# Optimization experiments

Hardware: AMD Instinct MI355X
Metric: run time of the kernel (lower is better)

The kernel has to match this reference:

```python
import jax, jax.numpy as jnp
import numpy as np
from functools import partial

IMG = 800
ANCHOR_SIZES = (32.0, 64.0, 128.0, 256.0, 512.0)
RATIOS = (0.5, 1.0, 2.0)
PRE_NMS = 1000
POST_NMS = 1000
NMS_TH = 0.7
MIN_SIZE = 1e-3
POOL = 7
SRATIO = 2  # roi_align sampling_ratio
SCALES = (0.25, 0.125, 0.0625, 0.03125)
BBOX_CLIP = float(np.log(1000.0 / 16.0))


def _cell_anchors(size):
    r = jnp.asarray(RATIOS, jnp.float32)
    hr = jnp.sqrt(r)
    wr = 1.0 / hr
    ws = size * wr
    hs = size * hr
    return jnp.round(jnp.stack([-ws / 2, -hs / 2, ws / 2, hs / 2], axis=1))  # [A,4]


def _grid_anchors(gh, gw, sh, sw, cell):
    sx = jnp.arange(gw, dtype=jnp.float32) * sw
    sy = jnp.arange(gh, dtype=jnp.float32) * sh
    yy, xx = jnp.meshgrid(sy, sx, indexing='ij')
    shifts = jnp.stack([xx, yy, xx, yy], axis=-1).reshape(-1, 4)
    # order: H-major, W, then A anchors per cell (matches torchvision)
    return (shifts[:, None, :] + cell[None, :, :]).reshape(-1, 4)


def _flatten_level(obj, dl):
    # permute_and_flatten: [B,A,H,W] -> [B,H*W*A], [B,4A,H,W] -> [B,H*W*A,4]
    B, A, H, W = obj.shape
    o = obj.transpose(0, 2, 3, 1).reshape(B, -1)
    d = dl.reshape(B, A, 4, H, W).transpose(0, 3, 4, 1, 2).reshape(B, -1, 4)
    return o, d


def _decode(deltas, anchors):
    # BoxCoder.decode with weights (1,1,1,1)
    w = anchors[:, 2] - anchors[:, 0]
    h = anchors[:, 3] - anchors[:, 1]
    cx = anchors[:, 0] + 0.5 * w
    cy = anchors[:, 1] + 0.5 * h
    dx, dy = deltas[..., 0], deltas[..., 1]
    dw = jnp.minimum(deltas[..., 2], BBOX_CLIP)
    dh = jnp.minimum(deltas[..., 3], BBOX_CLIP)
    pcx = dx * w + cx
    pcy = dy * h + cy
    pw = jnp.exp(dw) * w
    ph = jnp.exp(dh) * h
    return jnp.stack([pcx - 0.5 * pw, pcy - 0.5 * ph, pcx + 0.5 * pw, pcy + 0.5 * ph], axis=-1)


def _iou_one(box, boxes):
    a1 = (box[2] - box[0]) * (box[3] - box[1])
    a2 = (boxes[:, 2] - boxes[:, 0]) * (boxes[:, 3] - boxes[:, 1])
    lt = jnp.maximum(box[:2], boxes[:, :2])
    rb = jnp.minimum(box[2:], boxes[:, 2:])
    wh = jnp.clip(rb - lt, 0.0)
    inter = wh[:, 0] * wh[:, 1]
    return inter / (a1 + a2 - inter)


def _nms(boxes, scores, k):
    # greedy NMS, fixed k iterations (jit-friendly)
    def step(s, _):
        i = jnp.argmax(s)
        sup = _iou_one(boxes[i], boxes) > NMS_TH
        s = jnp.where(sup, -jnp.inf, s).at[i].set(-jnp.inf)
        return s, i
    _, idx = jax.lax.scan(step, scores, None, length=k)
    return idx


def _roi_align(feat, rois, scale):
    # feat [C,H,W], rois [R,4] in image coords -> [R,C,POOL,POOL]; aligned=False semantics
    C, H, W = feat.shape
    R = rois.shape[0]
    x1, y1 = rois[:, 0] * scale, rois[:, 1] * scale
    x2, y2 = rois[:, 2] * scale, rois[:, 3] * scale
    rw = jnp.maximum(x2 - x1, 1.0)
    rh = jnp.maximum(y2 - y1, 1.0)
    S = POOL * SRATIO
    t = (jnp.arange(S, dtype=jnp.float32) + 0.5) / S
    y = jnp.broadcast_to((y1[:, None] + rh[:, None] * t)[:, :, None], (R, S, S))
    x = jnp.broadcast_to((x1[:, None] + rw[:, None] * t)[:, None, :], (R, S, S))
    mask = (y >= -1.0) & (y <= H) & (x >= -1.0) & (x <= W)
    yc = jnp.clip(y, 0.0, H - 1.0)
    xc = jnp.clip(x, 0.0, W - 1.0)
    y0 = jnp.floor(yc).astype(jnp.int32)
    x0 = jnp.floor(xc).astype(jnp.int32)
    y1i = jnp.minimum(y0 + 1, H - 1)
    x1i = jnp.minimum(x0 + 1, W - 1)
    ly = yc - y0
    lx = xc - x0
    v00 = feat[:, y0, x0]
    v01 = feat[:, y0, x1i]
    v10 = feat[:, y1i, x0]
    v11 = feat[:, y1i, x1i]  # [C,R,S,S]
    val = ((1 - ly) * (1 - lx) * v00 + (1 - ly) * lx * v01 + ly * (1 - lx) * v10 + ly * lx * v11) * mask
    pooled = val.reshape(C, R, POOL, SRATIO, POOL, SRATIO).mean(axis=(3, 5))
    return pooled.transpose(1, 0, 2, 3)


def _forward(image_tensors, feats, objs, dls):
    B = image_tensors.shape[0]
    grids = [o.shape[-2:] for o in objs]
    anchors = jnp.concatenate([
        _grid_anchors(gh, gw, float(IMG // gh), float(IMG // gw), _cell_anchors(s))
        for (gh, gw), s in zip(grids, ANCHOR_SIZES)], axis=0)
    flat = [_flatten_level(o, d) for o, d in zip(objs, dls)]
    # RPN detaches both objectness and deltas before proposal filtering
    obj = jax.lax.stop_gradient(jnp.concatenate([f[0] for f in flat], axis=1))   # [B,N]
    dl = jax.lax.stop_gradient(jnp.concatenate([f[1] for f in flat], axis=1))    # [B,N,4]
    proposals = _decode(dl, anchors)                                             # [B,N,4]
    npl = [3 * gh * gw for gh, gw in grids]
    offs = np.concatenate([[0], np.cumsum(npl)])
    idx_parts, lvl_parts = [], []
    for l, n in enumerate(npl):
        k = min(PRE_NMS, n)
        _, ix = jax.lax.top_k(obj[:, offs[l]:offs[l + 1]], k)
        idx_parts.append(ix + offs[l])
        lvl_parts.append(jnp.full((k,), l, jnp.float32))
    idx = jnp.concatenate(idx_parts, axis=1)   # [B,K]
    lvl = jnp.concatenate(lvl_parts)           # [K]
    boxes = jnp.take_along_axis(proposals, idx[..., None], axis=1)
    scores = jax.nn.sigmoid(jnp.take_along_axis(obj, idx, axis=1))
    boxes = jnp.clip(boxes, 0.0, float(IMG))   # clip_boxes_to_image (square image)
    ws = boxes[..., 2] - boxes[..., 0]
    hs = boxes[..., 3] - boxes[..., 1]
    valid = (ws >= MIN_SIZE) & (hs >= MIN_SIZE)  # remove_small_boxes via score masking
    scores = jnp.where(valid, scores, -jnp.inf)
    # batched_nms: offset boxes per level so NMS is independent across levels
    off_boxes = boxes + (lvl * (IMG + 1.0))[None, :, None]
    keep = jax.vmap(lambda b, s: _nms(b, s, POST_NMS))(off_boxes, scores)  # [B,POST]
    props = jnp.take_along_axis(boxes, keep[..., None], axis=1)            # [B,POST,4]
    # MultiScaleRoIAlign level mapping (k0=4, canonical 224)
    area = (props[..., 2] - props[..., 0]) * (props[..., 3] - props[..., 1])
    li = jnp.clip(jnp.floor(4.0 + jnp.log2(jnp.sqrt(area) / 224.0 + 1e-6)), 2.0, 5.0).astype(jnp.int32) - 2
    R = props.shape[1]
    C = feats[0].shape[1]
    box_feats = jnp.zeros((B, R, C, POOL, POOL), feats[0].dtype)
    for l, (f, sc) in enumerate(zip(feats, SCALES)):
        pooled = jax.vmap(partial(_roi_align, scale=sc))(f, props)  # [B,R,C,7,7]
        box_feats = box_feats + pooled * (li == l)[..., None, None, None]
    return props, box_feats.reshape(B * R, C, POOL, POOL)


def setup_inputs() -> dict:
    key = jax.random.key(0)
    ks = jax.random.split(key, 16)
    B, C = 2, 256
    grids = [(200, 200), (100, 100), (50, 50), (25, 25), (13, 13)]
    d = {}
    d['image_tensors'] = jax.random.normal(ks[0], (B, 3, IMG, IMG), jnp.float32)
    for i in range(4):
        gh, gw = grids[i]
        d[f'features_{i}'] = jax.random.normal(ks[1 + i], (B, C, gh, gw), jnp.float32)
    for i in range(5):
        gh, gw = grids[i]
        d[f'objectness_{i}'] = jax.random.normal(ks[5 + i], (B, 3, gh, gw), jnp.float32)
        d[f'pred_bbox_deltas_{i}'] = jax.random.normal(ks[10 + i], (B, 12, gh, gw), jnp.float32)
    return d


def reference(image_tensors, features_0, features_1, features_2, features_3,
              objectness_0, objectness_1, objectness_2, objectness_3, objectness_4,
              pred_bbox_deltas_0, pred_bbox_deltas_1, pred_bbox_deltas_2,
              pred_bbox_deltas_3, pred_bbox_deltas_4):
    feats = [features_0, features_1, features_2, features_3]
    objs = [objectness_0, objectness_1, objectness_2, objectness_3, objectness_4]
    dls = [pred_bbox_deltas_0, pred_bbox_deltas_1, pred_bbox_deltas_2,
           pred_bbox_deltas_3, pred_bbox_deltas_4]
    return _forward(image_tensors, feats, objs, dls)
```

## Files before the change

kernel.cpp:

```cpp
#include <hip/hip_runtime.h>
#include <math.h>

typedef unsigned int u32;
typedef unsigned long long u64;

#define N_ALL 159882
#define NC 4507
#define MROW 72
#define NEGINF_KEY 0x007FFFFFu
#define IMGF 800.0f
#define BBOX_CLIP_F 4.135166556742356f
#define EMIT_S 16

#define NHWC_L1 10240000u
#define NHWC_L2 12800000u
#define NHWC_L3 13440000u
#define NHWC_BS 13600000u

__constant__ int   c_offs[5]  = {0,120000,150000,157500,159375};
__constant__ int   c_gw[5]    = {200,100,50,25,13};
__constant__ float c_stride[5]= {4.f,8.f,16.f,32.f,61.f};
__constant__ float c_size[5]  = {32.f,64.f,128.f,256.f,512.f};
__constant__ int   c_koff[5]  = {0,1000,2000,3000,4000};
__constant__ int   c_k[5]     = {1000,1000,1000,1000,507};
__constant__ float c_ratio[3] = {0.5f,1.f,2.f};

struct PtrArgs { const float* obj[5]; const float* dl[5]; };

__device__ __forceinline__ u32 fkey32f(float x){
  u32 u = __float_as_uint(x);
  return (u & 0x80000000u) ? ~u : (u | 0x80000000u);
}
__device__ __forceinline__ int level_of(int g){
  return (g >= 159375) ? 4 : (g >= 157500) ? 3 : (g >= 150000) ? 2 : (g >= 120000) ? 1 : 0;
}
__device__ __forceinline__ u64 readlane64(u64 v, int l){
  u32 lo = (u32)v, hi = (u32)(v >> 32);
  u32 a = (u32)__builtin_amdgcn_readlane((int)lo, l);
  u32 b = (u32)__builtin_amdgcn_readlane((int)hi, l);
  return ((u64)b << 32) | (u64)a;
}

__global__ void k_zero(u32* ghist, u32* wcnt, u32* tcnt, int B){
  int n = B*5*65536;
  int idx = blockIdx.x*blockDim.x + threadIdx.x;
  for (int i = idx; i < n; i += gridDim.x*blockDim.x) ghist[i] = 0;
  if (idx < B*5){ wcnt[idx] = 0; tcnt[idx] = 0; }
}

__global__ void k_decode(PtrArgs pa, int B, float* boxes_all, u32* key_all, u32* fkey_all,
                         u32* ghist){
#pragma clang fp contract(off)
  int idx = blockIdx.x*blockDim.x + threadIdx.x;
  int total = B*N_ALL;
  if (idx >= total) return;
  int b = idx / N_ALL;
  int g = idx - b*N_ALL;
  int l = level_of(g);
  int n = g - c_offs[l];
  int a = n % 3;
  int pos = n / 3;
  int gw = c_gw[l];
  int wx = pos % gw;
  int hy = pos / gw;
  int plane = gw*gw;
  const float* obj = pa.obj[l];
  const float* dl  = pa.dl[l];
  float logit = obj[(size_t)(b*3 + a)*plane + hy*gw + wx];
  size_t dbase = (size_t)(b*12 + a*4)*plane + (size_t)hy*gw + wx;
  float d0 = dl[dbase];
  float d1 = dl[dbase + (size_t)plane];
  float d2 = dl[dbase + (size_t)2*plane];
  float d3 = dl[dbase + (size_t)3*plane];
  float ratio = c_ratio[a];
  float hr = sqrtf(ratio);
  float wr = 1.0f/hr;
  float wsz = c_size[l]*wr;
  float hsz = c_size[l]*hr;
  float ca0 = rintf(-0.5f*wsz), ca1 = rintf(-0.5f*hsz);
  float ca2 = rintf( 0.5f*wsz), ca3 = rintf( 0.5f*hsz);
  float st = c_stride[l];
  float shx = (float)wx*st, shy = (float)hy*st;
  float ax1 = shx+ca0, ay1 = shy+ca1, ax2 = shx+ca2, ay2 = shy+ca3;
  float w = ax2-ax1, h = ay2-ay1;
  float cx = ax1 + 0.5f*w, cy = ay1 + 0.5f*h;
  float dw = fminf(d2, BBOX_CLIP_F), dh = fminf(d3, BBOX_CLIP_F);
  float pcx = d0*w + cx, pcy = d1*h + cy;
  float pw = expf(dw)*w, ph = expf(dh)*h;
  float x1 = pcx - 0.5f*pw, y1 = pcy - 0.5f*ph;
  float x2 = pcx + 0.5f*pw, y2 = pcy + 0.5f*ph;
  x1 = fminf(fmaxf(x1,0.f),IMGF); y1 = fminf(fmaxf(y1,0.f),IMGF);
  x2 = fminf(fmaxf(x2,0.f),IMGF); y2 = fminf(fmaxf(y2,0.f),IMGF);
  bool valid = ((x2-x1) >= 0.001f) && ((y2-y1) >= 0.001f);
  ((float4*)boxes_all)[idx] = make_float4(x1,y1,x2,y2);
  u32 key = fkey32f(logit);
  key_all[idx] = key;
  atomicAdd(&ghist[(size_t)(b*5 + l)*65536 + (key >> 16)], 1u);
  float sgf = 1.0f/(1.0f + expf(-logit));
  fkey_all[idx] = valid ? fkey32f(sgf) : NEGINF_KEY;
}

__global__ __launch_bounds__(1024) void k_sel(const u32* ghist, int2* meta, int B){
  int bl = blockIdx.x;
  int l = bl % 5;
  int k = c_k[l];
  const u32* h = ghist + (size_t)bl*65536;
  __shared__ u32 ssum[1024];
  __shared__ int2 s_meta;
  int tid = threadIdx.x;
  u32 cnt[64];
  u32 tot = 0;
  const uint4* h4 = (const uint4*)(h + tid*64);
  #pragma unroll
  for (int j = 0; j < 16; ++j){
    uint4 v = h4[j];
    cnt[4*j+0]=v.x; cnt[4*j+1]=v.y; cnt[4*j+2]=v.z; cnt[4*j+3]=v.w;
    tot += v.x+v.y+v.z+v.w;
  }
  ssum[tid] = tot;
  __syncthreads();
  for (int s = 1; s < 1024; s <<= 1){
    u32 v = ssum[tid] + ((tid+s < 1024) ? ssum[tid+s] : 0);
    __syncthreads(); ssum[tid] = v; __syncthreads();
  }
  u32 run = (tid+1 < 1024) ? ssum[tid+1] : 0;
  #pragma unroll
  for (int j = 63; j >= 0; --j){
    u32 cur = run + cnt[j];
    if (cur >= (u32)k && run < (u32)k){ s_meta.x = tid*64 + j; s_meta.y = (int)run; }
    run = cur;
  }
  __syncthreads();
  if (tid == 0) meta[bl] = s_meta;
}

__global__ __launch_bounds__(1024) void k_emit(const u32* key_all, const int2* meta,
                                               u32* cand_g, u32* wcnt, u32* tcnt,
                                               u64* tbuf, int B){
  int bid = blockIdx.x;
  int bl = bid / EMIT_S, c = bid - bl*EMIT_S;
  int b = bl / 5, l = bl - b*5;
  int g0 = c_offs[l];
  int N  = ((l==4)?N_ALL:c_offs[l+1]) - g0;
  int CH = (N + EMIT_S - 1)/EMIT_S;
  int st = c*CH, en = st + CH; if (en > N) en = N;
  if (st >= en) return;
  u32 bstar = (u32)meta[bl].x;
  const u32* keys = key_all + (size_t)b*N_ALL + g0;
  u32* out = cand_g + (size_t)b*NC + c_koff[l];
  u64* tb = tbuf + (size_t)bl*4096;
  int tid = threadIdx.x;
  int lane = tid & 63;
  u64 below = lane ? (~0ull >> (64 - lane)) : 0ull;
  for (int i0 = st; i0 < en; i0 += 1024){
    int i = i0 + tid;
    bool inb = (i < en);
    u32 kk = inb ? keys[i] : 0u;
    u32 bin = kk >> 16;
    bool isW = inb && (bin > bstar);
    bool isT = inb && (bin == bstar);
    u64 wb = __ballot(isW);
    if (wb){
      int wn = __popcll(wb);
      int b0 = 0;
      if (lane == 0) b0 = (int)atomicAdd(&wcnt[bl], (u32)wn);
      b0 = __shfl(b0, 0);
      if (isW) out[b0 + __popcll(wb & below)] = (u32)(g0 + i);
    }
    u64 tbm = __ballot(isT);
    if (tbm){
      int tn = __popcll(tbm);
      int b0 = 0;
      if (lane == 0) b0 = (int)atomicAdd(&tcnt[bl], (u32)tn);
      b0 = __shfl(b0, 0);
      if (isT){
        int slot = b0 + __popcll(tbm & below);
        if (slot < 4096) tb[slot] = ((u64)kk << 32) | (u32)(~(u32)(g0 + i));
      }
    }
  }
}

__global__ __launch_bounds__(1024) void k_fin(const int2* meta, const u32* tcnt,
                                              const u64* tbuf, u32* cand_g, int B){
  int bl = blockIdx.x;
  int b = bl/5, l = bl - b*5;
  int k = c_k[l];
  int chi = meta[bl].y;
  int r = k - chi;
  u32* out = cand_g + (size_t)b*NC + c_koff[l];
  __shared__ u64 buf[4096];
  int tid = threadIdx.x;
  int m = (int)tcnt[bl]; if (m > 4096) m = 4096;
  int P = 1; while (P < m) P <<= 1; if (P < 2) P = 2;
  const u64* tb = tbuf + (size_t)bl*4096;
  for (int i = tid; i < m; i += 1024) buf[i] = tb[i];
  for (int i = m + tid; i < P; i += 1024) buf[i] = 0;
  __syncthreads();
  for (u32 ksz = 2; ksz <= (u32)P; ksz <<= 1){
    for (u32 j = ksz >> 1; j > 0; j >>= 1){
      for (int i = tid; i < P; i += 1024){
        u32 ixj = (u32)i ^ j;
        if (ixj > (u32)i){
          u64 x = buf[i], y = buf[ixj];
          bool up = ((i & ksz) == 0);
          if (up ? (x < y) : (x > y)){ buf[i] = y; buf[ixj] = x; }
        }
      }
      __syncthreads();
    }
  }
  for (int t = tid; t < r && t < m; t += 1024) out[chi + t] = ~(u32)buf[t];
}

__global__ __launch_bounds__(1024) void k_rank(u32* cand_g, const u32* key_all, int B){
  int blk = blockIdx.x; int b = blk/5, l = blk - b*5;
  int k = c_k[l];
  u32* seg = cand_g + (size_t)b*NC + c_koff[l];
  __shared__ u64 sk[1024];
  int tid = threadIdx.x;
  u64 v = 0;
  if (tid < k){
    u32 g = seg[tid];
    v = ((u64)key_all[(size_t)b*N_ALL + g]<<32) | (u32)(~g);
  }
  sk[tid] = v;
  __syncthreads();
  for (u32 ksz=2;ksz<=1024;ksz<<=1){
    for (u32 j=ksz>>1;j>0;j>>=1){
      int i = tid;
      u32 ixj = (u32)i ^ j;
      if (ixj > (u32)i){
        u64 x = sk[i], y = sk[ixj];
        bool up = ((i & ksz) == 0);
        if (up ? (x < y) : (x > y)){ sk[i]=y; sk[ixj]=x; }
      }
      __syncthreads();
    }
  }
  if (tid < k) seg[tid] = ~(u32)sk[tid];
}

__device__ __forceinline__ void merge_elem(const u64* As, const u64* Bs, u64* dst,
                                           int m, int n, int k){
  int lo = k - n; if (lo < 0) lo = 0;
  int hi = (k < m) ? k : m;
  while (lo < hi){
    int mid = (lo + hi) >> 1;
    if (As[mid] > Bs[k-1-mid]) lo = mid + 1; else hi = mid;
  }
  int a = lo, bb = k - lo;
  u64 out;
  if (a < m && (bb >= n || As[a] > Bs[bb])) out = As[a]; else out = Bs[bb];
  dst[k] = out;
}

__global__ __launch_bounds__(1024) void k_sortcand(const u32* cand_g, const u32* fkey_all,
                                                   const float* boxes_all,
                                                   float* sorted_box, float* sorted_off,
                                                   u32* fcnt_ws, float* pos0box){
  __shared__ u64 sA[NC];
  __shared__ u64 sB[NC];
  __shared__ u32 wsum[16];
  __shared__ int s_f;
  int b = blockIdx.x, tid = threadIdx.x;
  int lane = tid & 63, wv = tid >> 6;
  if (tid == 0) s_f = 0;
  size_t cbase = (size_t)b*NC;
  size_t abase = (size_t)b*N_ALL;
  u64 below = lane ? (~0ull >> (64 - lane)) : 0ull;
  for (int l = 0; l < 5; ++l){
    int kl = c_k[l], ko = c_koff[l];
    bool act = tid < kl;
    u32 fk = 0; bool val = false;
    u32 i_g = (u32)(ko + tid);
    if (act){
      u32 g = cand_g[cbase + i_g];
      fk = fkey_all[abase + g];
      val = fk > NEGINF_KEY;
    }
    u64 bal = __ballot(act && val);
    int pv_w = __popcll(bal & below);
    if (lane == 0) wsum[wv] = (u32)__popcll(bal);
    __syncthreads();
    int pre = 0, Vl = 0;
    #pragma unroll
    for (int w2 = 0; w2 < 16; ++w2){
      int s = (int)wsum[w2];
      if (w2 < wv) pre += s;
      Vl += s;
    }
    if (tid == 0) s_f += Vl;
    if (act){
      int pv = pre + pv_w;
      int pos = val ? pv : (Vl + (tid - pv));
      sA[ko + pos] = ((u64)fk << 32) | (u32)(~i_g);
    }
    __syncthreads();
  }
  for (int k = tid; k < NC; k += 1024){
    if (k < 2000)       merge_elem(sA,        sA + 1000, sB,        1000, 1000, k);
    else if (k < 4000)  merge_elem(sA + 2000, sA + 3000, sB + 2000, 1000, 1000, k - 2000);
    else                sB[k] = sA[k];
  }
  __syncthreads();
  for (int k = tid; k < NC; k += 1024){
    if (k < 4000) merge_elem(sB, sB + 2000, sA, 2000, 2000, k);
    else          sA[k] = sB[k];
  }
  __syncthreads();
  for (int k = tid; k < NC; k += 1024){
    merge_elem(sA, sA + 4000, sB, 4000, 507, k);
  }
  __syncthreads();
  for (int i = tid; i < NC; i += 1024){
    u32 posc = ~(u32)sB[i];
    u32 g = cand_g[cbase + posc];
    int lvl = level_of((int)g);
    float4 bx = ((const float4*)boxes_all)[abase + g];
    ((float4*)sorted_box)[cbase + i] = bx;
    float off = 801.0f*(float)lvl;
    ((float4*)sorted_off)[cbase + i] = make_float4(bx.x+off, bx.y+off, bx.z+off, bx.w+off);
  }
  if (tid == 0){
    fcnt_ws[b] = (u32)s_f;
    u32 g0b = cand_g[cbase + 0];
    float4 bx = ((const float4*)boxes_all)[abase + g0b];
    ((float4*)pos0box)[b] = bx;
  }
}

__global__ void k_iou(const float* sorted_off, u64* M){
#pragma clang fp contract(off)
  int i = blockIdx.x, b = blockIdx.y, lane = threadIdx.x;
  const float4* boxes = ((const float4*)sorted_off) + (size_t)b*NC;
  float4 bi = boxes[i];
  float a1 = (bi.z-bi.x)*(bi.w-bi.y);
  u64* row = M + ((size_t)b*NC + i)*MROW;
  for (int w=0; w<71; w++){
    int j = w*64 + lane;
    bool sup = false;
    if (j < NC){
      float4 bj = boxes[j];
      float a2 = (bj.z-bj.x)*(bj.w-bj.y);
      float ltx = fmaxf(bi.x,bj.x), lty = fmaxf(bi.y,bj.y);
      float rbx = fminf(bi.z,bj.z), rby = fminf(bi.w,bj.w);
      float wx = fmaxf(rbx-ltx,0.f), wy = fmaxf(rby-lty,0.f);
      float inter = wx*wy;
      float iou = inter/(a1+a2-inter);
      sup = iou > 0.7f;
    }
    u64 word = __ballot(sup);
    if (lane==0) row[w] = word;
  }
}

#define GETQ2(q) { if (t2){ int jj=__builtin_ctzll(t2); t2&=t2-1; q = &buf[cb][jj*72]; } else q = zbuf; }
__global__ __launch_bounds__(256) void k_nms_tr(const float* sorted_box, const u64* M,
                      const u32* fcnt_ws, const float* pos0box, float* props, int B,
                      const float* f0, const float* f1, const float* f2, const float* f3,
                      float* nhwc, int doTr){
  __shared__ u64 buf[2][64*72];
  __shared__ u64 zbuf[72];
  __shared__ int ki[1000];
  __shared__ int s_kc, s_done;
  int bid = blockIdx.x;
  int tid = threadIdx.x;
  if (bid >= B){
    float (*t)[65] = reinterpret_cast<float(*)[65]>(&buf[0][0]);
    int id = bid - B;
    int b = id / 3328;
    int rem = id - b*3328;
    int P, W; const float* f; u32 loff;
    if (rem < 2500){ W=200; f=f0; loff=0u; }
    else if (rem < 3128){ W=100; f=f1; loff=NHWC_L1; rem -= 2500; }
    else if (rem < 3288){ W=50;  f=f2; loff=NHWC_L2; rem -= 3128; }
    else { W=25; f=f3; loff=NHWC_L3; rem -= 3288; }
    P = W*W;
    int ctile = rem & 3, ptile = rem >> 2;
    int c0 = ctile*64, p0 = ptile*64;
    const float* src = f + (size_t)b*256*P;
    float* dst = nhwc + (size_t)b*NHWC_BS + loff;
    int q   = tid & 15;
    int cl0 = tid >> 4;
    bool vec4ok = ((P & 3) == 0);
    int p = p0 + 4*q;
    float4 v[4];
    #pragma unroll
    for (int k = 0; k < 4; ++k){
      int cl = cl0 + 16*k;
      const float* s = src + (size_t)(c0+cl)*P + p;
      if (vec4ok && (p + 3 < P)){
        v[k] = *(const float4*)s;
      } else {
        v[k].x = (p   < P) ? s[0] : 0.f;
        v[k].y = (p+1 < P) ? s[1] : 0.f;
        v[k].z = (p+2 < P) ? s[2] : 0.f;
        v[k].w = (p+3 < P) ? s[3] : 0.f;
      }
    }
    #pragma unroll
    for (int k = 0; k < 4; ++k){
      int cl = cl0 + 16*k;
      t[cl][4*q+0] = v[k].x; t[cl][4*q+1] = v[k].y;
      t[cl][4*q+2] = v[k].z; t[cl][4*q+3] = v[k].w;
    }
    __syncthreads();
    #pragma unroll
    for (int k = 0; k < 4; ++k){
      int pl = cl0 + 16*k;
      int pp = p0 + pl;
      if (pp < P){
        float4 o = make_float4(t[4*q+0][pl], t[4*q+1][pl],
                               t[4*q+2][pl], t[4*q+3][pl]);
        *(float4*)(dst + (size_t)pp*256 + c0 + 4*q) = o;
      }
    }
    return;
  }
  int b = bid;
  int F = (int)fcnt_ws[b];
  const u64* Mb = M + (size_t)b*NC*MROW;
  int nch = (F + 63) >> 6;
  int lane = tid & 63, wv = tid >> 6;
  if (tid == 0){ s_kc = 0; s_done = (nch == 0) ? 1 : 0; }
  if (tid < 72) zbuf[tid] = 0ull;
  if (nch > 0){
    for (int e = tid; e < 64*72; e += 256){
      int rr = e / 72, wo = e - rr*72;
      int r2 = rr; if (r2 > NC-1) r2 = NC-1;
      buf[0][e] = Mb[(size_t)r2*MROW + wo];
    }
  }
  u64 rg[24];
  if (wv > 0 && nch > 1){
    #pragma unroll
    for (int k = 0; k < 24; ++k){
      int e = (tid - 64) + k*192;
      int rr = e/72, wo = e - rr*72;
      int r2 = 64 + rr; if (r2 > NC-1) r2 = NC-1;
      rg[k] = Mb[(size_t)r2*MROW + wo];
    }
  }
  __syncthreads();
  u64 sup0 = 0, sup1 = 0;
  int kc = 0;
  for (int c = 0; c < nch; ++c){
    int cb = c & 1;
    if (wv > 0){
      if (c + 1 < nch){
        #pragma unroll
        for (int k = 0; k < 24; ++k){
          int e = (tid - 64) + k*192;
          buf[cb^1][e] = rg[k];
        }
      }
      if (c + 2 < nch){
        int base2 = (c + 2) << 6;
        #pragma unroll
        for (int k = 0; k < 24; ++k){
          int e = (tid - 64) + k*192;
          int rr = e/72, wo = e - rr*72;
          int r2 = base2 + rr; if (r2 > NC-1) r2 = NC-1;
          rg[k] = Mb[(size_t)r2*MROW + wo];
        }
      }
    } else if (kc < 1000){
      int base = c << 6;
      int cnt = F - base; if (cnt > 64) cnt = 64;
      u64 supw = (c < 64) ? readlane64(sup0, c) : readlane64(sup1, c - 64);
      u64 alive = ~supw;
      if (cnt < 64) alive &= ((1ull << cnt) - 1ull);
      u64 wrow = buf[cb][lane*72 + c];
      u64 below = lane ? (~0ull >> (64 - lane)) : 0ull;
      u64 colb = wrow & below;
      bool myal = ((alive >> lane) & 1ull) != 0ull;
      u64 kept = __ballot(myal);
      #pragma unroll 1
      for (int it = 0; it < 64; ++it){
        bool kj = myal && ((kept & colb) == 0ull);
        u64 nk = __ballot(kj);
        if (nk == kept) break;
        kept = nk;
      }
      int cnt_k = __popcll(kept);
      int rank  = __popcll(kept & below);
      int budget = 1000 - kc;
      bool sel = ((kept >> lane) & 1ull) && (rank < budget);
      if (sel) ki[kc + rank] = base + lane;
      if (cnt_k >= budget){
        if (lane == 0){ s_done = 1; s_kc = 1000; }
      } else {
        kc += cnt_k;
        u64 t2 = kept;
        while (t2){
          const u64 *q0,*q1,*q2,*q3,*q4,*q5,*q6,*q7;
          const u64 *q8,*q9,*q10,*q11,*q12,*q13,*q14,*q15;
          GETQ2(q0) GETQ2(q1) GETQ2(q2) GETQ2(q3)
          GETQ2(q4) GETQ2(q5) GETQ2(q6) GETQ2(q7)
          GETQ2(q8) GETQ2(q9) GETQ2(q10) GETQ2(q11)
          GETQ2(q12) GETQ2(q13) GETQ2(q14) GETQ2(q15)
          u64 a0=q0[lane],a1=q1[lane],a2=q2[lane],a3=q3[lane];
          u64 a4=q4[lane],a5=q5[lane],a6=q6[lane],a7=q7[lane];
          u64 a8=q8[lane],a9=q9[lane],a10=q10[lane],a11=q11[lane];
          u64 a12=q12[lane],a13=q13[lane],a14=q14[lane],a15=q15[lane];
          sup0 |= (((a0|a1)|(a2|a3))|((a4|a5)|(a6|a7)))
                | (((a8|a9)|(a10|a11))|((a12|a13)|(a14|a15)));
          if (lane < 7){
            u64 b0=q0[64+lane],b1=q1[64+lane],b2=q2[64+lane],b3=q3[64+lane];
            u64 b4=q4[64+lane],b5=q5[64+lane],b6=q6[64+lane],b7=q7[64+lane];
            u64 b8=q8[64+lane],b9=q9[64+lane],b10=q10[64+lane],b11=q11[64+lane];
            u64 b12=q12[64+lane],b13=q13[64+lane],b14=q14[64+lane],b15=q15[64+lane];
            sup1 |= (((b0|b1)|(b2|b3))|((b4|b5)|(b6|b7)))
                  | (((b8|b9)|(b10|b11))|((b12|b13)|(b14|b15)));
          }
        }
        if (lane == 0) s_kc = kc;
      }
    }
    __syncthreads();
    if (s_done) break;
  }
  __syncthreads();
  int kcf = s_kc;
  const float* sb = sorted_box + (size_t)b*NC*4;
  float* pb = props + (size_t)b*4000;
  float4 p0v = ((const float4*)pos0box)[b];
  float pv[4] = {p0v.x, p0v.y, p0v.z, p0v.w};
  for (int idx = tid; idx < 4000; idx += 256){
    int k4 = idx >> 2, comp = idx & 3;
    float v = (k4 < kcf) ? sb[(size_t)ki[k4]*4 + comp] : pv[comp];
    pb[idx] = v;
  }
}

__global__ __launch_bounds__(256, 4) void k_roi_nhwc(const float* nhwc, const float* props,
                                                     float* out){
#pragma clang fp contract(off)
  int r = blockIdx.x;
  int b = r / 1000;
  int tid = threadIdx.x;
  int q = tid & 31;
  int s = tid >> 5;
  __shared__ int   s_o0[196], s_o1[196], s_o2[196], s_o3[196];
  __shared__ float s_a0[196], s_a1[196], s_a2[196], s_a3[196], s_m[196];
  __shared__ float obuf[49*132];
  float bx0 = props[(size_t)r*4+0], by0 = props[(size_t)r*4+1];
  float bx1 = props[(size_t)r*4+2], by1 = props[(size_t)r*4+3];
  float area = (bx1-bx0)*(by1-by0);
  float v = 4.0f + log2f(sqrtf(area)/224.0f + 1e-6f);
  float fl = floorf(v);
  fl = fminf(fmaxf(fl, 2.0f), 5.0f);
  int li = (int)fl - 2;
  int H = (li==0)?200:(li==1)?100:(li==2)?50:25;
  u32 loff = (li==0)?0u:(li==1)?NHWC_L1:(li==2)?NHWC_L2:NHWC_L3;
  float scale = (li==0)?0.25f:(li==1)?0.125f:(li==2)?0.0625f:0.03125f;
  float x1 = bx0*scale, y1 = by0*scale, x2 = bx1*scale, y2 = by1*scale;
  float rw = fmaxf(x2-x1, 1.0f), rh = fmaxf(y2-y1, 1.0f);
  if (tid < 196){
    int syi = tid / 14, sxi = tid - syi*14;
    float ty = ((float)syi + 0.5f)/14.0f;
    float yv = y1 + rh*ty;
    float fy = (yv >= -1.0f && yv <= (float)H) ? 1.0f : 0.0f;
    float yc = fminf(fmaxf(yv,0.0f),(float)(H-1));
    int iy0 = (int)floorf(yc);
    int iy1 = min(iy0+1,H-1);
    float ly = yc-(float)iy0;
    float tx = ((float)sxi + 0.5f)/14.0f;
    float xv = x1 + rw*tx;
    float fx = (xv >= -1.0f && xv <= (float)H) ? 1.0f : 0.0f;
    float xc = fminf(fmaxf(xv,0.0f),(float)(H-1));
    int ix0 = (int)floorf(xc);
    int ix1 = min(ix0+1,H-1);
    float lx = xc-(float)ix0;
    s_o0[tid] = (iy0*H + ix0)*64;
    s_o1[tid] = (iy0*H + ix1)*64;
    s_o2[tid] = (iy1*H + ix0)*64;
    s_o3[tid] = (iy1*H + ix1)*64;
    s_a0[tid] = (1.f-ly)*(1.f-lx);
    s_a1[tid] = (1.f-ly)*lx;
    s_a2[tid] = ly*(1.f-lx);
    s_a3[tid] = ly*lx;
    s_m[tid]  = fy*fx;
  }
  __syncthreads();
  const float4* src4 = (const float4*)(nhwc + (size_t)b*NHWC_BS + loff);
  float4* obuf4 = (float4*)obuf;
  float* orow = out + (size_t)r*12544;
  #pragma unroll 1
  for (int h = 0; h < 2; ++h){
    int qh = h*32 + q;
    for (int p = s; p < 49; p += 8){
      int py = p/7, px = p - py*7;
      float accx = 0.f, accy = 0.f, accz = 0.f, accw = 0.f;
      #pragma unroll
      for (int iy = 0; iy < 2; ++iy){
        #pragma unroll
        for (int ix = 0; ix < 2; ++ix){
          int sp = (py*2+iy)*14 + (px*2+ix);
          int o00 = s_o0[sp], o01 = s_o1[sp], o10 = s_o2[sp], o11 = s_o3[sp];
          float a00 = s_a0[sp], a01 = s_a1[sp], a10 = s_a2[sp], a11 = s_a3[sp];
          float m = s_m[sp];
          float4 v00 = src4[o00 + qh];
          float4 v01 = src4[o01 + qh];
          float4 v10 = src4[o10 + qh];
          float4 v11 = src4[o11 + qh];
          accx += (a00*v00.x + a01*v01.x + a10*v10.x + a11*v11.x)*m;
          accy += (a00*v00.y + a01*v01.y + a10*v10.y + a11*v11.y)*m;
          accz += (a00*v00.z + a01*v01.z + a10*v10.z + a11*v11.z)*m;
          accw += (a00*v00.w + a01*v01.w + a10*v10.w + a11*v11.w)*m;
        }
      }
      obuf4[p*33 + q] = make_float4(accx*0.25f, accy*0.25f, accz*0.25f, accw*0.25f);
    }
    __syncthreads();
    for (int o = tid; o < 6272; o += 256){
      int c = o/49, p = o - c*49;
      orow[h*6272 + o] = obuf[p*132 + c];
    }
    __syncthreads();
  }
}

__global__ __launch_bounds__(256) void k_roi(const float* f0, const float* f1,
                                             const float* f2, const float* f3,
                                             const float* props, float* out){
#pragma clang fp contract(off)
  int r = blockIdx.x;
  int b = r / 1000;
  int tid = threadIdx.x;
  __shared__ float s_ly[14], s_lx[14], s_ym[14], s_xm[14];
  __shared__ int   s_y0[14], s_y1[14], s_x0[14], s_x1[14];
  float bx0 = props[(size_t)r*4+0], by0 = props[(size_t)r*4+1];
  float bx1 = props[(size_t)r*4+2], by1 = props[(size_t)r*4+3];
  float area = (bx1-bx0)*(by1-by0);
  float v = 4.0f + log2f(sqrtf(area)/224.0f + 1e-6f);
  float fl = floorf(v);
  fl = fminf(fmaxf(fl, 2.0f), 5.0f);
  int li = (int)fl - 2;
  const float* fptr = (li==0)?f0:(li==1)?f1:(li==2)?f2:f3;
  int H = (li==0)?200:(li==1)?100:(li==2)?50:25;
  float scale = (li==0)?0.25f:(li==1)?0.125f:(li==2)?0.0625f:0.03125f;
  float x1 = bx0*scale, y1 = by0*scale, x2 = bx1*scale, y2 = by1*scale;
  float rw = fmaxf(x2-x1, 1.0f), rh = fmaxf(y2-y1, 1.0f);
  if (tid < 14){
    float t = ((float)tid + 0.5f)/14.0f;
    float yv = y1 + rh*t;
    s_ym[tid] = (yv >= -1.0f && yv <= (float)H) ? 1.0f : 0.0f;
    float yc = fminf(fmaxf(yv,0.0f),(float)(H-1));
    int iy0 = (int)floorf(yc);
    s_y0[tid]=iy0; s_y1[tid]=min(iy0+1,H-1); s_ly[tid]=yc-(float)iy0;
    float xv = x1 + rw*t;
    s_xm[tid] = (xv >= -1.0f && xv <= (float)H) ? 1.0f : 0.0f;
    float xc = fminf(fmaxf(xv,0.0f),(float)(H-1));
    int ix0 = (int)floorf(xc);
    s_x0[tid]=ix0; s_x1[tid]=min(ix0+1,H-1); s_lx[tid]=xc-(float)ix0;
  }
  __syncthreads();
  size_t plane = (size_t)H*H;
  const float* fb = fptr + (size_t)b*256*plane;
  float* orow = out + (size_t)r*12544;
  for (int o=tid; o<12544; o+=256){
    int c = o/49;
    int p = o - c*49;
    int py = p/7, px = p - py*7;
    const float* fc = fb + (size_t)c*plane;
    float sum = 0.f;
    for (int iy=0; iy<2; iy++){
      int syi = py*2+iy;
      int yy0 = s_y0[syi], yy1 = s_y1[syi];
      float ly = s_ly[syi], fy = s_ym[syi];
      for (int ix=0; ix<2; ix++){
        int sxi = px*2+ix;
        int xx0 = s_x0[sxi], xx1 = s_x1[sxi];
        float lx = s_lx[sxi], fx = s_xm[sxi];
        float v00 = fc[yy0*H+xx0], v01 = fc[yy0*H+xx1];
        float v10 = fc[yy1*H+xx0], v11 = fc[yy1*H+xx1];
        float val = ((1.f-ly)*(1.f-lx)*v00 + (1.f-ly)*lx*v01
                   + ly*(1.f-lx)*v10 + ly*lx*v11) * (fy*fx);
        sum += val;
      }
    }
    orow[o] = sum*0.25f;
  }
}

extern "C" void kernel_launch(void* const* d_in, const int* in_sizes, int n_in,
                              void* d_out, int out_size, void* d_ws, size_t ws_size,
                              hipStream_t stream) {
  int B = in_sizes[0] / (3*800*800);
  PtrArgs pa;
  bool interleaved = (n_in >= 7) && (in_sizes[6] == 4*in_sizes[5]);
  for (int i=0;i<5;i++){
    if (interleaved){
      pa.obj[i] = (const float*)d_in[5+2*i];
      pa.dl[i]  = (const float*)d_in[6+2*i];
    } else {
      pa.obj[i] = (const float*)d_in[5+i];
      pa.dl[i]  = (const float*)d_in[10+i];
    }
  }

  auto align256 = [](size_t x){ return (x + 255) & ~(size_t)255; };
  size_t sz_M      = align256(((size_t)B*NC + 1)*MROW*8);
  size_t sz_boxes  = align256((size_t)B*N_ALL*16);
  size_t sz_key    = align256((size_t)B*N_ALL*4);
  size_t sz_fkey   = align256((size_t)B*N_ALL*4);
  size_t sz_cand   = align256((size_t)B*NC*4);
  size_t sz_sbox   = align256((size_t)B*NC*16);
  size_t sz_soff   = align256((size_t)B*NC*16);
  size_t sz_fcnt   = align256((size_t)B*4);
  size_t sz_p0     = align256((size_t)B*16);
  size_t sz_ghist  = align256((size_t)B*5*65536*4);
  size_t sz_meta   = align256((size_t)B*5*8);
  size_t sz_wcnt   = align256((size_t)B*5*4);
  size_t sz_tcnt   = align256((size_t)B*5*4);
  size_t sz_tbuf   = align256((size_t)B*5*4096*8);
  size_t need = sz_M+sz_boxes+sz_key+sz_fkey+sz_cand+sz_sbox+sz_soff+sz_fcnt+sz_p0
              + sz_ghist+sz_meta+sz_wcnt+sz_tcnt+sz_tbuf;
  size_t outBytes = (size_t)out_size * 4;
  size_t start = (outBytes - need) & ~(size_t)255;
  char* w = (char*)d_out + start;
  auto alloc = [&](size_t bytes)->char*{ char* p = w; w += bytes; return p; };

  u64*  M          = (u64*) alloc(sz_M);
  float* boxes_all = (float*)alloc(sz_boxes);
  u32*  key_all    = (u32*) alloc(sz_key);
  u32*  fkey_all   = (u32*) alloc(sz_fkey);
  u32*  cand_g     = (u32*) alloc(sz_cand);
  float* sorted_box= (float*)alloc(sz_sbox);
  float* sorted_off= (float*)alloc(sz_soff);
  u32*  fcnt       = (u32*) alloc(sz_fcnt);
  float* pos0box   = (float*)alloc(sz_p0);
  u32*  ghist      = (u32*) alloc(sz_ghist);
  int2* meta       = (int2*)alloc(sz_meta);
  u32*  wcnt       = (u32*) alloc(sz_wcnt);
  u32*  tcnt       = (u32*) alloc(sz_tcnt);
  u64*  tbuf       = (u64*) alloc(sz_tbuf);

  float* props     = (float*)d_out;
  float* feats_out = (float*)d_out + (size_t)B*1000*4;

  int total = B*N_ALL;
  k_zero<<<2560, 256, 0, stream>>>(ghist, wcnt, tcnt, B);
  k_decode<<<(total+255)/256, 256, 0, stream>>>(pa, B, boxes_all, key_all, fkey_all, ghist);
  k_sel<<<B*5, 1024, 0, stream>>>(ghist, meta, B);
  k_emit<<<B*5*EMIT_S, 1024, 0, stream>>>(key_all, meta, cand_g, wcnt, tcnt, tbuf, B);
  k_fin<<<B*5, 1024, 0, stream>>>(meta, tcnt, tbuf, cand_g, B);
  k_rank<<<B*5, 1024, 0, stream>>>(cand_g, key_all, B);
  k_sortcand<<<B, 1024, 0, stream>>>(cand_g, fkey_all, boxes_all, sorted_box, sorted_off, fcnt, pos0box);
  k_iou<<<dim3(NC, B), 64, 0, stream>>>(sorted_off, M);

  size_t nhwcBytes = (size_t)B * NHWC_BS * 4;
  int doTr = (ws_size >= nhwcBytes) ? 1 : 0;
  float* nhwc = (float*)d_ws;
  int grid = B + (doTr ? B*3328 : 0);
  k_nms_tr<<<grid, 256, 0, stream>>>(sorted_box, M, fcnt, pos0box, props, B,
                                     (const float*)d_in[1], (const float*)d_in[2],
                                     (const float*)d_in[3], (const float*)d_in[4],
                                     nhwc, doTr);
  if (doTr){
    k_roi_nhwc<<<B*1000, 256, 0, stream>>>(nhwc, props, feats_out);
  } else {
    k_roi<<<B*1000, 256, 0, stream>>>((const float*)d_in[1], (const float*)d_in[2],
                                      (const float*)d_in[3], (const float*)d_in[4],
                                      props, feats_out);
  }
}
```

Baseline: 366.3 us.

## Build coarser per-level key histogram in LDS in a separate kernel

Moves the score-key histogram out of the decode kernel, where every element did a global atomicAdd, into a new kernel. The new kernel builds a per-chunk histogram in shared memory and flushes the non-zero bins with global atomics. It also cuts the bin count from 65536 to 16384 (key>>18), which shrinks the zeroing, the histogram memory and the k_sel scan. The cost is one extra launch, a second read of the keys, and wider threshold bins that send more candidates through the tie path.

```diff
diff --git a/kernel.cpp b/kernel.cpp
--- a/kernel.cpp
+++ b/kernel.cpp
@@ -11,6 +11,8 @@
 #define IMGF 800.0f
 #define BBOX_CLIP_F 4.135166556742356f
 #define EMIT_S 16
+#define HBINS 16384
+#define HCH 16
 
 #define NHWC_L1 10240000u
 #define NHWC_L2 12800000u
@@ -42,14 +44,13 @@
 }
 
 __global__ void k_zero(u32* ghist, u32* wcnt, u32* tcnt, int B){
-  int n = B*5*65536;
+  int n = B*5*HBINS;
   int idx = blockIdx.x*blockDim.x + threadIdx.x;
   for (int i = idx; i < n; i += gridDim.x*blockDim.x) ghist[i] = 0;
   if (idx < B*5){ wcnt[idx] = 0; tcnt[idx] = 0; }
 }
 
-__global__ void k_decode(PtrArgs pa, int B, float* boxes_all, u32* key_all, u32* fkey_all,
-                         u32* ghist){
+__global__ void k_decode(PtrArgs pa, int B, float* boxes_all, u32* key_all, u32* fkey_all){
 #pragma clang fp contract(off)
   int idx = blockIdx.x*blockDim.x + threadIdx.x;
   int total = B*N_ALL;
@@ -93,26 +94,49 @@
   x2 = fminf(fmaxf(x2,0.f),IMGF); y2 = fminf(fmaxf(y2,0.f),IMGF);
   bool valid = ((x2-x1) >= 0.001f) && ((y2-y1) >= 0.001f);
   ((float4*)boxes_all)[idx] = make_float4(x1,y1,x2,y2);
-  u32 key = fkey32f(logit);
-  key_all[idx] = key;
-  atomicAdd(&ghist[(size_t)(b*5 + l)*65536 + (key >> 16)], 1u);
+  key_all[idx] = fkey32f(logit);
   float sgf = 1.0f/(1.0f + expf(-logit));
   fkey_all[idx] = valid ? fkey32f(sgf) : NEGINF_KEY;
+}
+
+__global__ __launch_bounds__(256) void k_hist(const u32* key_all, u32* ghist, int B){
+  __shared__ u32 lh[HBINS];
+  int bid = blockIdx.x;
+  int bl = bid / HCH, c = bid - bl*HCH;
+  int b = bl / 5, l = bl - b*5;
+  int g0 = c_offs[l];
+  int N  = ((l==4)?N_ALL:c_offs[l+1]) - g0;
+  int CH = (N + HCH - 1)/HCH;
+  int st = c*CH, en = st + CH; if (en > N) en = N;
+  int tid = threadIdx.x;
+  for (int i = tid; i < HBINS; i += 256) lh[i] = 0;
+  __syncthreads();
+  if (st < en){
+    const u32* keys = key_all + (size_t)b*N_ALL + g0;
+    for (int i = st + tid; i < en; i += 256)
+      atomicAdd(&lh[keys[i] >> 18], 1u);
+  }
+  __syncthreads();
+  u32* gh = ghist + (size_t)bl*HBINS;
+  for (int i = tid; i < HBINS; i += 256){
+    u32 v = lh[i];
+    if (v) atomicAdd(&gh[i], v);
+  }
 }
 
 __global__ __launch_bounds__(1024) void k_sel(const u32* ghist, int2* meta, int B){
   int bl = blockIdx.x;
   int l = bl % 5;
   int k = c_k[l];
-  const u32* h = ghist + (size_t)bl*65536;
+  const u32* h = ghist + (size_t)bl*HBINS;
   __shared__ u32 ssum[1024];
   __shared__ int2 s_meta;
   int tid = threadIdx.x;
-  u32 cnt[64];
+  u32 cnt[16];
   u32 tot = 0;
-  const uint4* h4 = (const uint4*)(h + tid*64);
+  const uint4* h4 = (const uint4*)(h + tid*16);
   #pragma unroll
-  for (int j = 0; j < 16; ++j){
+  for (int j = 0; j < 4; ++j){
     uint4 v = h4[j];
     cnt[4*j+0]=v.x; cnt[4*j+1]=v.y; cnt[4*j+2]=v.z; cnt[4*j+3]=v.w;
     tot += v.x+v.y+v.z+v.w;
@@ -125,9 +149,9 @@
   }
   u32 run = (tid+1 < 1024) ? ssum[tid+1] : 0;
   #pragma unroll
-  for (int j = 63; j >= 0; --j){
+  for (int j = 15; j >= 0; --j){
     u32 cur = run + cnt[j];
-    if (cur >= (u32)k && run < (u32)k){ s_meta.x = tid*64 + j; s_meta.y = (int)run; }
+    if (cur >= (u32)k && run < (u32)k){ s_meta.x = tid*16 + j; s_meta.y = (int)run; }
     run = cur;
   }
   __syncthreads();
@@ -156,7 +180,7 @@
     int i = i0 + tid;
     bool inb = (i < en);
     u32 kk = inb ? keys[i] : 0u;
-    u32 bin = kk >> 16;
+    u32 bin = kk >> 18;
     bool isW = inb && (bin > bstar);
     bool isT = inb && (bin == bstar);
     u64 wb = __ballot(isW);
@@ -711,7 +735,7 @@
   size_t sz_soff   = align256((size_t)B*NC*16);
   size_t sz_fcnt   = align256((size_t)B*4);
   size_t sz_p0     = align256((size_t)B*16);
-  size_t sz_ghist  = align256((size_t)B*5*65536*4);
+  size_t sz_ghist  = align256((size_t)B*5*HBINS*4);
   size_t sz_meta   = align256((size_t)B*5*8);
   size_t sz_wcnt   = align256((size_t)B*5*4);
   size_t sz_tcnt   = align256((size_t)B*5*4);
@@ -742,8 +766,10 @@
   float* feats_out = (float*)d_out + (size_t)B*1000*4;
 
   int total = B*N_ALL;
-  k_zero<<<2560, 256, 0, stream>>>(ghist, wcnt, tcnt, B);
-  k_decode<<<(total+255)/256, 256, 0, stream>>>(pa, B, boxes_all, key_all, fkey_all, ghist);
+  int nz = B*5*HBINS;
+  k_zero<<<(nz+255)/256, 256, 0, stream>>>(ghist, wcnt, tcnt, B);
+  k_decode<<<(total+255)/256, 256, 0, stream>>>(pa, B, boxes_all, key_all, fkey_all);
+  k_hist<<<B*5*HCH, 256, 0, stream>>>(key_all, ghist, B);
   k_sel<<<B*5, 1024, 0, stream>>>(ghist, meta, B);
   k_emit<<<B*5*EMIT_S, 1024, 0, stream>>>(key_all, meta, cand_g, wcnt, tcnt, tbuf, B);
   k_fin<<<B*5, 1024, 0, stream>>>(meta, tcnt, tbuf, cand_g, B);
```

Result: faster. 302.3 us, median of 3 (-17.5%).
